# Optimization experiments

Hardware: AMD Instinct MI355X
Metric: run time of the kernel (lower is better)

Reference implementation:

```python
import jax, jax.numpy as jnp
import numpy as np

N_NODES = 100000
AVG_DEG = 32
E_UND = N_NODES * AVG_DEG // 2   # 1.6M undirected edges
E_DIR = 2 * E_UND                # 3.2M directed edges
Q = 4                            # number of communities
NUM_ITER = 10                    # max_num_iter in bp_params


def setup_inputs() -> dict:
    key = jax.random.key(0)
    k1, k2, k3, k4 = jax.random.split(key, 4)
    src_u = jax.random.randint(k1, (E_UND,), 0, N_NODES)
    dst_u = jax.random.randint(k2, (E_UND,), 0, N_NODES)
    # symmetric directed edge list: [forward block | reverse block]
    edge_index = jnp.stack([
        jnp.concatenate([src_u, dst_u]),
        jnp.concatenate([dst_u, src_u]),
    ]).astype(jnp.int64)
    w_u = jax.random.uniform(k3, (E_UND,), dtype=jnp.float32)
    edge_attr = jnp.concatenate([w_u, w_u])  # symmetric weights
    msg_init = jax.random.uniform(k4, (E_DIR, Q), dtype=jnp.float32) + 0.1
    # critical beta for q groups, mean degree c: log(q/(sqrt(c)-1)+1)
    beta = jnp.asarray(np.log(Q / (np.sqrt(AVG_DEG) - 1.0) + 1.0), dtype=jnp.float32)
    return {"edge_index": edge_index, "edge_attr": edge_attr,
            "msg_init": msg_init, "beta": beta, "num_nodes": N_NODES}


def _bp_forward(edge_index, edge_attr, msg_init, beta, num_nodes):
    q = msg_init.shape[1]
    E = edge_index.shape[1]
    e_und = E // 2
    src, dst = edge_index[0], edge_index[1]
    # reverse-edge permutation: edge e <-> e +/- e_und
    rev = jnp.concatenate([jnp.arange(e_und) + e_und, jnp.arange(e_und)])

    two_m = jnp.sum(edge_attr)                                   # = 2m (directed sum)
    deg = jax.ops.segment_sum(edge_attr, src, num_segments=num_nodes)  # weighted degree [N]
    expm1_bw = jnp.expm1(beta * edge_attr)[:, None]              # [E,1]

    psi0 = msg_init / jnp.sum(msg_init, axis=-1, keepdims=True)  # normalized cavity msgs [E,q]
    h0 = jnp.zeros((q,), dtype=msg_init.dtype)                   # external field

    def step(carry, _):
        psi, h = carry
        L = jnp.log1p(psi * expm1_bw)                            # [E,q] log(1 + psi*(e^{bw}-1))
        S = jax.ops.segment_sum(L, dst, num_segments=num_nodes)  # [N,q] incoming log-products
        marg = jax.nn.softmax(h[None, :] + S, axis=-1)           # node marginals [N,q]
        h_new = -(beta / two_m) * jnp.sum(deg[:, None] * marg, axis=0)  # [q]
        # cavity update for edge i->j: all incoming at i except reverse edge j->i
        msg_log = h_new[None, :] + S[src] - L[rev]
        psi_new = jax.nn.softmax(msg_log, axis=-1)
        return (psi_new, h_new), None

    (psi, h), _ = jax.lax.scan(step, (psi0, h0), None, length=NUM_ITER)

    # final node marginals s
    L = jnp.log1p(psi * expm1_bw)
    S = jax.ops.segment_sum(L, dst, num_segments=num_nodes)
    s = jax.nn.softmax(h[None, :] + S, axis=-1)                  # [N,q]

    # modularity: Q = (1/2m) sum_e w_e <s_i, s_j> - sum_t (sum_i d_i s_it / 2m)^2
    link = jnp.sum(edge_attr[:, None] * s[src] * s[dst]) / two_m
    comm_deg = jnp.sum(deg[:, None] * s, axis=0) / two_m         # [q]
    q_mod = link - jnp.sum(comm_deg * comm_deg)
    return s, q_mod


def reference(edge_index, edge_attr, msg_init, beta, num_nodes):
    return _bp_forward(edge_index, edge_attr, msg_init, beta, num_nodes)
```

## Files before the change

kernel.cpp:

```cpp
#include <hip/hip_runtime.h>


#define NBLK 256
#define QD 4
#define SENT 0x7fffffff

__device__ __forceinline__ float wave_red(float v) {
#pragma unroll
  for (int o = 32; o > 0; o >>= 1) v += __shfl_down(v, o, 64);
  return v;
}

__device__ __forceinline__ void atomicMulF(float* addr, float val) {
  unsigned int old = __float_as_uint(*addr), assumed;
  do {
    assumed = old;
    float nv = __uint_as_float(assumed) * val;
    old = atomicCAS((unsigned int*)addr, assumed, __float_as_uint(nv));
  } while (old != assumed);
}

__global__ void hist_rank(const int* __restrict__ ei, int* __restrict__ cnt,
                          int* __restrict__ rank, int E) {
  int G = gridDim.x * blockDim.x;
  int e[8], d[8];
#pragma unroll
  for (int j = 0; j < 8; ++j) {
    e[j] = blockIdx.x * blockDim.x + threadIdx.x + j * G;
    d[j] = (e[j] < E) ? ei[E + e[j]] : 0;
  }
#pragma unroll
  for (int j = 0; j < 8; ++j)
    if (e[j] < E) rank[e[j]] = atomicAdd(&cnt[d[j]], 1);
}

__global__ void scanA(const int* __restrict__ cnt, int* __restrict__ out,
                      int* __restrict__ bsum, int N) {
  __shared__ int lds[256];
  int base = blockIdx.x * 1024 + threadIdx.x * 4;
  int v0 = (base + 0 < N) ? cnt[base + 0] : 0;
  int v1 = (base + 1 < N) ? cnt[base + 1] : 0;
  int v2 = (base + 2 < N) ? cnt[base + 2] : 0;
  int v3 = (base + 3 < N) ? cnt[base + 3] : 0;
  lds[threadIdx.x] = v0 + v1 + v2 + v3;
  __syncthreads();
  for (int off = 1; off < 256; off <<= 1) {
    int x = (threadIdx.x >= off) ? lds[threadIdx.x - off] : 0;
    __syncthreads();
    if (threadIdx.x >= off) lds[threadIdx.x] += x;
    __syncthreads();
  }
  int excl = (threadIdx.x == 0) ? 0 : lds[threadIdx.x - 1];
  if (threadIdx.x == 255) bsum[blockIdx.x] = lds[255];
  if (base + 0 < N) out[base + 0] = excl;
  if (base + 1 < N) out[base + 1] = excl + v0;
  if (base + 2 < N) out[base + 2] = excl + v0 + v1;
  if (base + 3 < N) out[base + 3] = excl + v0 + v1 + v2;
}

__global__ void scanB(int* __restrict__ bsum, int NB) {
  __shared__ int lds[256];
  int v = (threadIdx.x < NB) ? bsum[threadIdx.x] : 0;
  lds[threadIdx.x] = v;
  __syncthreads();
  for (int off = 1; off < 256; off <<= 1) {
    int x = (threadIdx.x >= off) ? lds[threadIdx.x - off] : 0;
    __syncthreads();
    if (threadIdx.x >= off) lds[threadIdx.x] += x;
    __syncthreads();
  }
  int excl = (threadIdx.x == 0) ? 0 : lds[threadIdx.x - 1];
  if (threadIdx.x < NB) bsum[threadIdx.x] = excl;
}

__global__ void scanC(int* __restrict__ rowStart, const int* __restrict__ bsum,
                      int N, int E) {
  int i = blockIdx.x * blockDim.x + threadIdx.x;
  if (i < N) rowStart[i] += bsum[i >> 10];
  if (i == 0) rowStart[N] = E;
}

__global__ void scatter_inc(const int* __restrict__ ei, const int* __restrict__ rowStart,
                            const int* __restrict__ rank, int* __restrict__ inc, int E) {
  int G = gridDim.x * blockDim.x;
#pragma unroll
  for (int j = 0; j < 4; ++j) {
    int e = blockIdx.x * blockDim.x + threadIdx.x + j * G;
    if (e < E) {
      int d = ei[E + e];
      inc[rowStart[d] + rank[e]] = e;
    }
  }
}

__global__ void build_nodeOf(const int* __restrict__ rowStart, int* __restrict__ nodeOf,
                             int N) {
  int n = blockIdx.x * blockDim.x + threadIdx.x;
  if (n >= N) return;
  int s = rowStart[n], e = rowStart[n + 1];
  for (int k = s; k < e; ++k) nodeOf[k] = n;
}

__global__ void setup_pairs(const float* __restrict__ w, const float* __restrict__ msg,
                            const float* __restrict__ beta_p, float* __restrict__ F,
                            float* __restrict__ em_buf, double* __restrict__ two_m,
                            int Eh) {
  __shared__ float blk[4];
  int t = blockIdx.x * blockDim.x + threadIdx.x;
  float tw = 0.f;
  if (t < Eh) {
    float beta = beta_p[0];
    float wv = w[t];
    tw = 2.f * wv;
    float em = expm1f(beta * wv);
    em_buf[t] = em;
    float4 m1 = *reinterpret_cast<const float4*>(&msg[(size_t)t * QD]);
    float4 m2 = *reinterpret_cast<const float4*>(&msg[((size_t)t + Eh) * QD]);
    float i1 = em / (m1.x + m1.y + m1.z + m1.w);
    float i2 = em / (m2.x + m2.y + m2.z + m2.w);
    float4 F1 = make_float4(fmaf(m1.x, i1, 1.f), fmaf(m1.y, i1, 1.f),
                            fmaf(m1.z, i1, 1.f), fmaf(m1.w, i1, 1.f));
    float4 F2 = make_float4(fmaf(m2.x, i2, 1.f), fmaf(m2.y, i2, 1.f),
                            fmaf(m2.z, i2, 1.f), fmaf(m2.w, i2, 1.f));
    *reinterpret_cast<float4*>(&F[(size_t)t * QD]) = F1;
    *reinterpret_cast<float4*>(&F[((size_t)t + Eh) * QD]) = F2;
  }
  tw = wave_red(tw);
  int wid = threadIdx.x >> 6;
  if ((threadIdx.x & 63) == 0) blk[wid] = tw;
  __syncthreads();
  if (threadIdx.x == 0)
    atomicAdd(two_m, (double)(blk[0] + blk[1] + blk[2] + blk[3]));
}

__global__ void fillP(float* __restrict__ P, int n4) {
  int i = blockIdx.x * blockDim.x + threadIdx.x;
  if (i < n4) P[i] = 1.0f;
}

template <int NC, bool PROD, int NW>
__global__ void gather_seg(const int* __restrict__ inc, const int* __restrict__ nodeOf,
                           const float* __restrict__ src, float* __restrict__ out,
                           int E) {
  const int lane = threadIdx.x & 63;
  const int wid = threadIdx.x >> 6;
  const long long base = ((long long)blockIdx.x * (blockDim.x >> 6) + wid) * (NW * 64);
  if (base >= E) return;
  const float IDENT = PROD ? 1.f : 0.f;
  int n[NW], idx[NW];
  float v[NW][NC];
#pragma unroll
  for (int w = 0; w < NW; ++w) {
    long long k = base + w * 64 + lane;
    n[w] = (k < E) ? nodeOf[k] : SENT;
    idx[w] = (k < E) ? inc[k] : 0;
  }
#pragma unroll
  for (int w = 0; w < NW; ++w) {
    long long k = base + w * 64 + lane;
    if (k < E) {
      if constexpr (NC == 4) {
        float4 t = *reinterpret_cast<const float4*>(&src[(size_t)idx[w] * 4]);
        v[w][0] = t.x; v[w][1] = t.y; v[w][2] = t.z; v[w][3] = t.w;
      } else {
        v[w][0] = src[idx[w]];
      }
    } else {
#pragma unroll
      for (int c = 0; c < NC; ++c) v[w][c] = IDENT;
    }
  }
  int n00 = __shfl(n[0], 0, 64);
  int prevn = (base > 0) ? nodeOf[base - 1] : -1;
  const int incomplete = (prevn == n00) ? n00 : -1;
  int nwf[NW];
#pragma unroll
  for (int w = 0; w < NW - 1; ++w) nwf[w] = __shfl(n[w + 1], 0, 64);
  nwf[NW - 1] = (base + NW * 64 < E) ? nodeOf[base + NW * 64] : -1;

  float cv[NC];
#pragma unroll
  for (int c = 0; c < NC; ++c) cv[c] = IDENT;
  int cn = -1;
#pragma unroll
  for (int w = 0; w < NW; ++w) {
    int nn = n[w];
#pragma unroll
    for (int d = 1; d < 64; d <<= 1) {
      int pn = __shfl_up(nn, d, 64);
      float pv[NC];
#pragma unroll
      for (int c = 0; c < NC; ++c) pv[c] = __shfl_up(v[w][c], d, 64);
      if (lane >= d && pn == nn) {
#pragma unroll
        for (int c = 0; c < NC; ++c) {
          if constexpr (PROD) v[w][c] *= pv[c]; else v[w][c] += pv[c];
        }
      }
    }
    if (nn == cn) {
#pragma unroll
      for (int c = 0; c < NC; ++c) {
        if constexpr (PROD) v[w][c] *= cv[c]; else v[w][c] += cv[c];
      }
    }
    int nnext = __shfl_down(nn, 1, 64);
    if (lane == 63) nnext = nwf[w];
    bool segend = (nn != SENT) && (nnext != nn);
    if (segend) {
      if (nn == incomplete) {
#pragma unroll
        for (int c = 0; c < NC; ++c) {
          if constexpr (PROD) atomicMulF(&out[(size_t)nn * NC + c], v[w][c]);
          else atomicAdd(&out[(size_t)nn * NC + c], v[w][c]);
        }
      } else {
        if constexpr (NC == 4) {
          *reinterpret_cast<float4*>(&out[(size_t)nn * 4]) =
              make_float4(v[w][0], v[w][1], v[w][2], v[w][3]);
        } else {
          out[nn] = v[w][0];
        }
      }
    }
    int last_n = __shfl(nn, 63, 64);
    float lv[NC];
#pragma unroll
    for (int c = 0; c < NC; ++c) lv[c] = __shfl(v[w][c], 63, 64);
    bool last_end = (nwf[w] != last_n) || (last_n == SENT);
    if (last_end) {
      cn = -1;
#pragma unroll
      for (int c = 0; c < NC; ++c) cv[c] = IDENT;
    } else {
      cn = last_n;
#pragma unroll
      for (int c = 0; c < NC; ++c) cv[c] = lv[c];
    }
  }
  if (cn != -1 && lane == 0) {
#pragma unroll
    for (int c = 0; c < NC; ++c) {
      if constexpr (PROD) atomicMulF(&out[(size_t)cn * NC + c], cv[c]);
      else atomicAdd(&out[(size_t)cn * NC + c], cv[c]);
    }
  }
}

__global__ void node_post(const float* __restrict__ P, const float* __restrict__ deg,
                          const double* __restrict__ hsum_prev, double* __restrict__ hsum_new,
                          const float* __restrict__ beta_p, const double* __restrict__ two_m,
                          int N) {
  __shared__ float blk[4][4];
  int n = blockIdx.x * blockDim.x + threadIdx.x;
  float scale = -beta_p[0] / (float)two_m[0];
  float e0 = expf(scale * (float)hsum_prev[0]);
  float e1 = expf(scale * (float)hsum_prev[1]);
  float e2 = expf(scale * (float)hsum_prev[2]);
  float e3 = expf(scale * (float)hsum_prev[3]);
  float a0 = 0.f, a1 = 0.f, a2 = 0.f, a3 = 0.f;
  if (n < N) {
    float4 Pv = *reinterpret_cast<const float4*>(&P[(size_t)n * QD]);
    float m0 = e0 * Pv.x, m1 = e1 * Pv.y, m2 = e2 * Pv.z, m3 = e3 * Pv.w;
    float dinv = deg[n] / (m0 + m1 + m2 + m3);
    a0 = m0 * dinv; a1 = m1 * dinv; a2 = m2 * dinv; a3 = m3 * dinv;
  }
  a0 = wave_red(a0); a1 = wave_red(a1); a2 = wave_red(a2); a3 = wave_red(a3);
  int wid = threadIdx.x >> 6;
  if ((threadIdx.x & 63) == 0) {
    blk[wid][0] = a0; blk[wid][1] = a1; blk[wid][2] = a2; blk[wid][3] = a3;
  }
  __syncthreads();
  if (threadIdx.x < 4) {
    float s = blk[0][threadIdx.x] + blk[1][threadIdx.x] + blk[2][threadIdx.x] +
              blk[3][threadIdx.x];
    atomicAdd(&hsum_new[threadIdx.x], (double)s);
  }
}

__global__ void node_post_final(const float* __restrict__ P, const float* __restrict__ deg,
                                const double* __restrict__ hsum, const float* __restrict__ beta_p,
                                const double* __restrict__ two_m, float* __restrict__ out_s,
                                double* __restrict__ comm_raw, int N) {
  __shared__ float blk[4][4];
  int n = blockIdx.x * blockDim.x + threadIdx.x;
  float scale = -beta_p[0] / (float)two_m[0];
  float e0 = expf(scale * (float)hsum[0]);
  float e1 = expf(scale * (float)hsum[1]);
  float e2 = expf(scale * (float)hsum[2]);
  float e3 = expf(scale * (float)hsum[3]);
  float a0 = 0.f, a1 = 0.f, a2 = 0.f, a3 = 0.f;
  if (n < N) {
    float4 Pv = *reinterpret_cast<const float4*>(&P[(size_t)n * QD]);
    float m0 = e0 * Pv.x, m1 = e1 * Pv.y, m2 = e2 * Pv.z, m3 = e3 * Pv.w;
    float inv = 1.f / (m0 + m1 + m2 + m3);
    float4 s = make_float4(m0 * inv, m1 * inv, m2 * inv, m3 * inv);
    *reinterpret_cast<float4*>(&out_s[(size_t)n * QD]) = s;
    float d = deg[n];
    a0 = d * s.x; a1 = d * s.y; a2 = d * s.z; a3 = d * s.w;
  }
  a0 = wave_red(a0); a1 = wave_red(a1); a2 = wave_red(a2); a3 = wave_red(a3);
  int wid = threadIdx.x >> 6;
  if ((threadIdx.x & 63) == 0) {
    blk[wid][0] = a0; blk[wid][1] = a1; blk[wid][2] = a2; blk[wid][3] = a3;
  }
  __syncthreads();
  if (threadIdx.x < 4) {
    float s = blk[0][threadIdx.x] + blk[1][threadIdx.x] + blk[2][threadIdx.x] +
              blk[3][threadIdx.x];
    atomicAdd(&comm_raw[threadIdx.x], (double)s);
  }
}

__global__ void edge_fuse(const int* __restrict__ ei, const float* __restrict__ em_buf,
                          const float* __restrict__ P, float* __restrict__ F,
                          const double* __restrict__ hsum, const float* __restrict__ beta_p,
                          const double* __restrict__ two_m, int E, int Eh) {
  int t = blockIdx.x * blockDim.x + threadIdx.x;
  if (t >= Eh) return;
  float scale = -beta_p[0] / (float)two_m[0];
  float e0 = expf(scale * (float)hsum[0]);
  float e1 = expf(scale * (float)hsum[1]);
  float e2 = expf(scale * (float)hsum[2]);
  float e3 = expf(scale * (float)hsum[3]);
  int s1 = ei[t];
  int d1 = ei[E + t];
  float em = em_buf[t];
  float4 F1 = *reinterpret_cast<const float4*>(&F[(size_t)t * QD]);
  float4 F2 = *reinterpret_cast<const float4*>(&F[((size_t)t + Eh) * QD]);
  float4 Ps = *reinterpret_cast<const float4*>(&P[(size_t)s1 * QD]);
  float4 Pd = *reinterpret_cast<const float4*>(&P[(size_t)d1 * QD]);
  {
    float a01 = F2.x * F2.y, a23 = F2.z * F2.w;
    float x0 = F2.y * a23, x1 = F2.x * a23, x2 = a01 * F2.w, x3 = a01 * F2.z;
    float n0 = e0 * Ps.x * x0, n1 = e1 * Ps.y * x1;
    float n2 = e2 * Ps.z * x2, n3 = e3 * Ps.w * x3;
    float tt = em / (n0 + n1 + n2 + n3);
    float4 Fn = make_float4(fmaf(n0, tt, 1.f), fmaf(n1, tt, 1.f),
                            fmaf(n2, tt, 1.f), fmaf(n3, tt, 1.f));
    *reinterpret_cast<float4*>(&F[(size_t)t * QD]) = Fn;
  }
  {
    float a01 = F1.x * F1.y, a23 = F1.z * F1.w;
    float x0 = F1.y * a23, x1 = F1.x * a23, x2 = a01 * F1.w, x3 = a01 * F1.z;
    float n0 = e0 * Pd.x * x0, n1 = e1 * Pd.y * x1;
    float n2 = e2 * Pd.z * x2, n3 = e3 * Pd.w * x3;
    float tt = em / (n0 + n1 + n2 + n3);
    float4 Fn = make_float4(fmaf(n0, tt, 1.f), fmaf(n1, tt, 1.f),
                            fmaf(n2, tt, 1.f), fmaf(n3, tt, 1.f));
    *reinterpret_cast<float4*>(&F[((size_t)t + Eh) * QD]) = Fn;
  }
}

__global__ void edge_final(const int* __restrict__ ei, const float* __restrict__ w,
                           const float* __restrict__ out_s,
                           double* __restrict__ link_raw, int E, int Eh) {
  __shared__ float blk[4];
  int G = gridDim.x * blockDim.x;
  float c = 0.f;
  for (int t = blockIdx.x * blockDim.x + threadIdx.x; t < Eh; t += G) {
    int s1 = ei[t];
    int d1 = ei[E + t];
    float4 a = *reinterpret_cast<const float4*>(&out_s[(size_t)s1 * QD]);
    float4 b = *reinterpret_cast<const float4*>(&out_s[(size_t)d1 * QD]);
    float dot = a.x * b.x + a.y * b.y + a.z * b.z + a.w * b.w;
    c += 2.f * w[t] * dot;
  }
  c = wave_red(c);
  int wid = threadIdx.x >> 6;
  if ((threadIdx.x & 63) == 0) blk[wid] = c;
  __syncthreads();
  if (threadIdx.x == 0)
    atomicAdd(link_raw, (double)(blk[0] + blk[1] + blk[2] + blk[3]));
}

__global__ void finalize(const double* __restrict__ scal, float* __restrict__ out_q) {
  double tm = scal[0];
  double link = scal[1] / tm;
  double acc = 0.0;
#pragma unroll
  for (int k = 0; k < QD; ++k) {
    double c = scal[2 + k] / tm;
    acc += c * c;
  }
  out_q[0] = (float)(link - acc);
}

extern "C" void kernel_launch(void* const* d_in, const int* in_sizes, int n_in,
                              void* d_out, int out_size, void* d_ws, size_t ws_size,
                              hipStream_t stream) {
  const int* ei = (const int*)d_in[0];
  const float* w = (const float*)d_in[1];
  const float* msg = (const float*)d_in[2];
  const float* beta_p = (const float*)d_in[3];

  const int E = in_sizes[1];
  const int Eh = E / 2;
  const int N = (out_size - 1) / QD;

  char* p = (char*)d_ws;
  double* scal = (double*)p;
  size_t off = 512;
  int* cnt = (int*)(p + off); off += (size_t)N * 4;
  int* rowStart = (int*)(p + off); off += (size_t)(N + 1) * 4;
  off = (off + 127) & ~(size_t)127;
  int* bsum = (int*)(p + off); off += 1024;
  int* inc = (int*)(p + off); off += (size_t)E * 4;
  float* deg = (float*)(p + off); off += (size_t)N * 4;
  off = (off + 15) & ~(size_t)15;
  float* P = (float*)(p + off); off += (size_t)N * QD * 4;
  float* em = (float*)(p + off); off += (size_t)Eh * 4;
  off = (off + 15) & ~(size_t)15;
  float* F = (float*)(p + off); off += (size_t)E * QD * 4;
  int* rank = (int*)F;
  int* nodeOf = (int*)(p + off); off += (size_t)E * 4;
  (void)ws_size;

  double* hs = scal + 6;
  const int gEdir = (E + NBLK - 1) / NBLK;
  const int gE = (Eh + NBLK - 1) / NBLK;
  const int gN = (N + NBLK - 1) / NBLK;
  const int gH = (E + NBLK * 8 - 1) / (NBLK * 8);
  const int gSc = (E + NBLK * 4 - 1) / (NBLK * 4);
  const int gWp = (E + 2047) / 2048;
  const int gWd = (E + 1023) / 1024;
  const int gF = (4 * N + NBLK - 1) / NBLK;
  const int NBscan = (N + 1023) / 1024;

  hipMemsetAsync(scal, 0, 512, stream);
  hipMemsetAsync(cnt, 0, (size_t)N * 4, stream);
  hipMemsetAsync(deg, 0, (size_t)N * 4, stream);

  hist_rank<<<gH, NBLK, 0, stream>>>(ei, cnt, rank, E);
  scanA<<<NBscan, 256, 0, stream>>>(cnt, rowStart, bsum, N);
  scanB<<<1, 256, 0, stream>>>(bsum, NBscan);
  scanC<<<(N + NBLK) / NBLK, NBLK, 0, stream>>>(rowStart, bsum, N, E);
  scatter_inc<<<gSc, NBLK, 0, stream>>>(ei, rowStart, rank, inc, E);
  build_nodeOf<<<gN, NBLK, 0, stream>>>(rowStart, nodeOf, N);

  setup_pairs<<<gE, NBLK, 0, stream>>>(w, msg, beta_p, F, em, scal, Eh);
  gather_seg<1, false, 4><<<gWd, NBLK, 0, stream>>>(inc, nodeOf, w, deg, E);

  float* out_s = (float*)d_out;
  for (int i = 1; i <= 10; ++i) {
    fillP<<<gF, NBLK, 0, stream>>>(P, 4 * N);
    gather_seg<4, true, 8><<<gWp, NBLK, 0, stream>>>(inc, nodeOf, F, P, E);
    node_post<<<gN, NBLK, 0, stream>>>(P, deg, hs + 4 * (i - 1), hs + 4 * i,
                                       beta_p, scal, N);
    edge_fuse<<<gE, NBLK, 0, stream>>>(ei, em, P, F, hs + 4 * i, beta_p, scal, E, Eh);
  }
  fillP<<<gF, NBLK, 0, stream>>>(P, 4 * N);
  gather_seg<4, true, 8><<<gWp, NBLK, 0, stream>>>(inc, nodeOf, F, P, E);
  node_post_final<<<gN, NBLK, 0, stream>>>(P, deg, hs + 40, beta_p, scal,
                                           out_s, scal + 2, N);
  edge_final<<<512, NBLK, 0, stream>>>(ei, w, out_s, scal + 1, E, Eh);
  finalize<<<1, 1, 0, stream>>>(scal, out_s + (size_t)N * QD);
}
```

Measured before the change: 1.719 ms.

## Split F gather into separate permute pass and double edge work per thread

Adds a gatherF kernel that permutes edge messages into destination-sorted order (Fg) with 8 independent loads per thread. The segmented product then reads Fg sequentially instead of through the incidence index, but only when the workspace is large enough. edge_fuse now processes two edge pairs per thread over half the grid, and scatter_inc handles 8 edges per thread. The cost is an extra full E×4 float write and read per iteration plus an extra kernel launch.

```diff
diff --git a/kernel.cpp b/kernel.cpp
--- a/kernel.cpp
+++ b/kernel.cpp
@@ -84,7 +84,7 @@
                             const int* __restrict__ rank, int* __restrict__ inc, int E) {
   int G = gridDim.x * blockDim.x;
 #pragma unroll
-  for (int j = 0; j < 4; ++j) {
+  for (int j = 0; j < 8; ++j) {
     int e = blockIdx.x * blockDim.x + threadIdx.x + j * G;
     if (e < E) {
       int d = ei[E + e];
@@ -138,7 +138,25 @@
   if (i < n4) P[i] = 1.0f;
 }
 
-template <int NC, bool PROD, int NW>
+__global__ void gatherF(const int* __restrict__ inc, const float* __restrict__ F,
+                        float* __restrict__ Fg, int E) {
+  int G = gridDim.x * blockDim.x;
+  int k[8], id[8];
+#pragma unroll
+  for (int j = 0; j < 8; ++j) {
+    k[j] = blockIdx.x * blockDim.x + threadIdx.x + j * G;
+    id[j] = (k[j] < E) ? inc[k[j]] : 0;
+  }
+  float4 v[8];
+#pragma unroll
+  for (int j = 0; j < 8; ++j)
+    v[j] = *reinterpret_cast<const float4*>(&F[(size_t)id[j] * QD]);
+#pragma unroll
+  for (int j = 0; j < 8; ++j)
+    if (k[j] < E) *reinterpret_cast<float4*>(&Fg[(size_t)k[j] * QD]) = v[j];
+}
+
+template <int NC, bool PROD, int NW, bool SEQIDX>
 __global__ void gather_seg(const int* __restrict__ inc, const int* __restrict__ nodeOf,
                            const float* __restrict__ src, float* __restrict__ out,
                            int E) {
@@ -153,7 +171,8 @@
   for (int w = 0; w < NW; ++w) {
     long long k = base + w * 64 + lane;
     n[w] = (k < E) ? nodeOf[k] : SENT;
-    idx[w] = (k < E) ? inc[k] : 0;
+    if constexpr (SEQIDX) idx[w] = (int)k;
+    else idx[w] = (k < E) ? inc[k] : 0;
   }
 #pragma unroll
   for (int w = 0; w < NW; ++w) {
@@ -316,40 +335,52 @@
                           const float* __restrict__ P, float* __restrict__ F,
                           const double* __restrict__ hsum, const float* __restrict__ beta_p,
                           const double* __restrict__ two_m, int E, int Eh) {
-  int t = blockIdx.x * blockDim.x + threadIdx.x;
-  if (t >= Eh) return;
+  int G = gridDim.x * blockDim.x;
+  int t0 = blockIdx.x * blockDim.x + threadIdx.x;
+  int t1 = t0 + G;
   float scale = -beta_p[0] / (float)two_m[0];
   float e0 = expf(scale * (float)hsum[0]);
   float e1 = expf(scale * (float)hsum[1]);
   float e2 = expf(scale * (float)hsum[2]);
   float e3 = expf(scale * (float)hsum[3]);
-  int s1 = ei[t];
-  int d1 = ei[E + t];
-  float em = em_buf[t];
-  float4 F1 = *reinterpret_cast<const float4*>(&F[(size_t)t * QD]);
-  float4 F2 = *reinterpret_cast<const float4*>(&F[((size_t)t + Eh) * QD]);
-  float4 Ps = *reinterpret_cast<const float4*>(&P[(size_t)s1 * QD]);
-  float4 Pd = *reinterpret_cast<const float4*>(&P[(size_t)d1 * QD]);
-  {
-    float a01 = F2.x * F2.y, a23 = F2.z * F2.w;
-    float x0 = F2.y * a23, x1 = F2.x * a23, x2 = a01 * F2.w, x3 = a01 * F2.z;
-    float n0 = e0 * Ps.x * x0, n1 = e1 * Ps.y * x1;
-    float n2 = e2 * Ps.z * x2, n3 = e3 * Ps.w * x3;
-    float tt = em / (n0 + n1 + n2 + n3);
-    float4 Fn = make_float4(fmaf(n0, tt, 1.f), fmaf(n1, tt, 1.f),
-                            fmaf(n2, tt, 1.f), fmaf(n3, tt, 1.f));
-    *reinterpret_cast<float4*>(&F[(size_t)t * QD]) = Fn;
-  }
-  {
-    float a01 = F1.x * F1.y, a23 = F1.z * F1.w;
-    float x0 = F1.y * a23, x1 = F1.x * a23, x2 = a01 * F1.w, x3 = a01 * F1.z;
-    float n0 = e0 * Pd.x * x0, n1 = e1 * Pd.y * x1;
-    float n2 = e2 * Pd.z * x2, n3 = e3 * Pd.w * x3;
-    float tt = em / (n0 + n1 + n2 + n3);
-    float4 Fn = make_float4(fmaf(n0, tt, 1.f), fmaf(n1, tt, 1.f),
-                            fmaf(n2, tt, 1.f), fmaf(n3, tt, 1.f));
-    *reinterpret_cast<float4*>(&F[((size_t)t + Eh) * QD]) = Fn;
-  }
+  int s1a = 0, d1a = 0, s1b = 0, d1b = 0;
+  float ema = 0.f, emb = 0.f;
+  if (t0 < Eh) { s1a = ei[t0]; d1a = ei[E + t0]; ema = em_buf[t0]; }
+  if (t1 < Eh) { s1b = ei[t1]; d1b = ei[E + t1]; emb = em_buf[t1]; }
+  float4 F1a, F2a, F1b, F2b, Psa, Pda, Psb, Pdb;
+  if (t0 < Eh) {
+    F1a = *reinterpret_cast<const float4*>(&F[(size_t)t0 * QD]);
+    F2a = *reinterpret_cast<const float4*>(&F[((size_t)t0 + Eh) * QD]);
+    Psa = *reinterpret_cast<const float4*>(&P[(size_t)s1a * QD]);
+    Pda = *reinterpret_cast<const float4*>(&P[(size_t)d1a * QD]);
+  }
+  if (t1 < Eh) {
+    F1b = *reinterpret_cast<const float4*>(&F[(size_t)t1 * QD]);
+    F2b = *reinterpret_cast<const float4*>(&F[((size_t)t1 + Eh) * QD]);
+    Psb = *reinterpret_cast<const float4*>(&P[(size_t)s1b * QD]);
+    Pdb = *reinterpret_cast<const float4*>(&P[(size_t)d1b * QD]);
+  }
+#define CAV(Fr, Pn, em, dstp)                                            \
+  {                                                                      \
+    float a01 = (Fr).x * (Fr).y, a23 = (Fr).z * (Fr).w;                  \
+    float x0 = (Fr).y * a23, x1 = (Fr).x * a23;                          \
+    float x2 = a01 * (Fr).w, x3 = a01 * (Fr).z;                          \
+    float n0 = e0 * (Pn).x * x0, n1 = e1 * (Pn).y * x1;                  \
+    float n2 = e2 * (Pn).z * x2, n3 = e3 * (Pn).w * x3;                  \
+    float tt = (em) / (n0 + n1 + n2 + n3);                               \
+    *reinterpret_cast<float4*>(dstp) =                                   \
+        make_float4(fmaf(n0, tt, 1.f), fmaf(n1, tt, 1.f),                \
+                    fmaf(n2, tt, 1.f), fmaf(n3, tt, 1.f));               \
+  }
+  if (t0 < Eh) {
+    CAV(F2a, Psa, ema, &F[(size_t)t0 * QD]);
+    CAV(F1a, Pda, ema, &F[((size_t)t0 + Eh) * QD]);
+  }
+  if (t1 < Eh) {
+    CAV(F2b, Psb, emb, &F[(size_t)t1 * QD]);
+    CAV(F1b, Pdb, emb, &F[((size_t)t1 + Eh) * QD]);
+  }
+#undef CAV
 }
 
 __global__ void edge_final(const int* __restrict__ ei, const float* __restrict__ w,
@@ -414,14 +445,17 @@
   float* F = (float*)(p + off); off += (size_t)E * QD * 4;
   int* rank = (int*)F;
   int* nodeOf = (int*)(p + off); off += (size_t)E * 4;
-  (void)ws_size;
+  off = (off + 15) & ~(size_t)15;
+  float* Fg = (float*)(p + off); off += (size_t)E * QD * 4;
+  const bool twophase = ws_size >= off;
 
   double* hs = scal + 6;
   const int gEdir = (E + NBLK - 1) / NBLK;
   const int gE = (Eh + NBLK - 1) / NBLK;
+  const int gE2 = (Eh / 2 + NBLK - 1) / NBLK + 1;
   const int gN = (N + NBLK - 1) / NBLK;
   const int gH = (E + NBLK * 8 - 1) / (NBLK * 8);
-  const int gSc = (E + NBLK * 4 - 1) / (NBLK * 4);
+  const int gGF = (E + NBLK * 8 - 1) / (NBLK * 8);
   const int gWp = (E + 2047) / 2048;
   const int gWd = (E + 1023) / 1024;
   const int gF = (4 * N + NBLK - 1) / NBLK;
@@ -435,22 +469,27 @@
   scanA<<<NBscan, 256, 0, stream>>>(cnt, rowStart, bsum, N);
   scanB<<<1, 256, 0, stream>>>(bsum, NBscan);
   scanC<<<(N + NBLK) / NBLK, NBLK, 0, stream>>>(rowStart, bsum, N, E);
-  scatter_inc<<<gSc, NBLK, 0, stream>>>(ei, rowStart, rank, inc, E);
+  scatter_inc<<<gH, NBLK, 0, stream>>>(ei, rowStart, rank, inc, E);
   build_nodeOf<<<gN, NBLK, 0, stream>>>(rowStart, nodeOf, N);
 
   setup_pairs<<<gE, NBLK, 0, stream>>>(w, msg, beta_p, F, em, scal, Eh);
-  gather_seg<1, false, 4><<<gWd, NBLK, 0, stream>>>(inc, nodeOf, w, deg, E);
+  gather_seg<1, false, 4, false><<<gWd, NBLK, 0, stream>>>(inc, nodeOf, w, deg, E);
 
   float* out_s = (float*)d_out;
-  for (int i = 1; i <= 10; ++i) {
+  for (int i = 1; i <= 11; ++i) {
     fillP<<<gF, NBLK, 0, stream>>>(P, 4 * N);
-    gather_seg<4, true, 8><<<gWp, NBLK, 0, stream>>>(inc, nodeOf, F, P, E);
-    node_post<<<gN, NBLK, 0, stream>>>(P, deg, hs + 4 * (i - 1), hs + 4 * i,
-                                       beta_p, scal, N);
-    edge_fuse<<<gE, NBLK, 0, stream>>>(ei, em, P, F, hs + 4 * i, beta_p, scal, E, Eh);
-  }
-  fillP<<<gF, NBLK, 0, stream>>>(P, 4 * N);
-  gather_seg<4, true, 8><<<gWp, NBLK, 0, stream>>>(inc, nodeOf, F, P, E);
+    if (twophase) {
+      gatherF<<<gGF, NBLK, 0, stream>>>(inc, F, Fg, E);
+      gather_seg<4, true, 8, true><<<gWp, NBLK, 0, stream>>>(inc, nodeOf, Fg, P, E);
+    } else {
+      gather_seg<4, true, 8, false><<<gWp, NBLK, 0, stream>>>(inc, nodeOf, F, P, E);
+    }
+    if (i <= 10) {
+      node_post<<<gN, NBLK, 0, stream>>>(P, deg, hs + 4 * (i - 1), hs + 4 * i,
+                                         beta_p, scal, N);
+      edge_fuse<<<gE2, NBLK, 0, stream>>>(ei, em, P, F, hs + 4 * i, beta_p, scal, E, Eh);
+    }
+  }
   node_post_final<<<gN, NBLK, 0, stream>>>(P, deg, hs + 40, beta_p, scal,
                                            out_s, scal + 2, N);
   edge_final<<<512, NBLK, 0, stream>>>(ei, w, out_s, scal + 1, E, Eh);
```

After: 1.954 ms. 1.14x slower.

## Store cavity messages in CSR order with double-buffered per-slot metadata

Applied to the files above, without the earlier changes.

Edge messages F are now kept in destination-sorted CSR order, so the product-gather reads F sequentially instead of through the inc indirection. A setup kernel precomputes, per CSR slot, the source node, the edge weight term and the slot of the reverse edge. A new cavity kernel writes F_new in CSR order using the reverse slot, with ping-pong buffers to avoid read/write hazards. The cost is extra workspace and random reads of the reverse edge's F in the cavity step; the old path stays as a fallback when the workspace is too small.

```diff
diff --git a/kernel.cpp b/kernel.cpp
--- a/kernel.cpp
+++ b/kernel.cpp
@@ -80,15 +80,18 @@
   if (i == 0) rowStart[N] = E;
 }
 
-__global__ void scatter_inc(const int* __restrict__ ei, const int* __restrict__ rowStart,
-                            const int* __restrict__ rank, int* __restrict__ inc, int E) {
+__global__ void scatter_inc2(const int* __restrict__ ei, const int* __restrict__ rowStart,
+                             const int* __restrict__ rank, int* __restrict__ inc,
+                             int* __restrict__ csrPos, int E) {
   int G = gridDim.x * blockDim.x;
 #pragma unroll
   for (int j = 0; j < 4; ++j) {
     int e = blockIdx.x * blockDim.x + threadIdx.x + j * G;
     if (e < E) {
       int d = ei[E + e];
-      inc[rowStart[d] + rank[e]] = e;
+      int pos = rowStart[d] + rank[e];
+      inc[pos] = e;
+      csrPos[e] = pos;
     }
   }
 }
@@ -104,7 +107,7 @@
 __global__ void setup_pairs(const float* __restrict__ w, const float* __restrict__ msg,
                             const float* __restrict__ beta_p, float* __restrict__ F,
                             float* __restrict__ em_buf, double* __restrict__ two_m,
-                            int Eh) {
+                            int Eh, int writeF) {
   __shared__ float blk[4];
   int t = blockIdx.x * blockDim.x + threadIdx.x;
   float tw = 0.f;
@@ -114,16 +117,18 @@
     tw = 2.f * wv;
     float em = expm1f(beta * wv);
     em_buf[t] = em;
-    float4 m1 = *reinterpret_cast<const float4*>(&msg[(size_t)t * QD]);
-    float4 m2 = *reinterpret_cast<const float4*>(&msg[((size_t)t + Eh) * QD]);
-    float i1 = em / (m1.x + m1.y + m1.z + m1.w);
-    float i2 = em / (m2.x + m2.y + m2.z + m2.w);
-    float4 F1 = make_float4(fmaf(m1.x, i1, 1.f), fmaf(m1.y, i1, 1.f),
-                            fmaf(m1.z, i1, 1.f), fmaf(m1.w, i1, 1.f));
-    float4 F2 = make_float4(fmaf(m2.x, i2, 1.f), fmaf(m2.y, i2, 1.f),
-                            fmaf(m2.z, i2, 1.f), fmaf(m2.w, i2, 1.f));
-    *reinterpret_cast<float4*>(&F[(size_t)t * QD]) = F1;
-    *reinterpret_cast<float4*>(&F[((size_t)t + Eh) * QD]) = F2;
+    if (writeF) {
+      float4 m1 = *reinterpret_cast<const float4*>(&msg[(size_t)t * QD]);
+      float4 m2 = *reinterpret_cast<const float4*>(&msg[((size_t)t + Eh) * QD]);
+      float i1 = em / (m1.x + m1.y + m1.z + m1.w);
+      float i2 = em / (m2.x + m2.y + m2.z + m2.w);
+      float4 F1 = make_float4(fmaf(m1.x, i1, 1.f), fmaf(m1.y, i1, 1.f),
+                              fmaf(m1.z, i1, 1.f), fmaf(m1.w, i1, 1.f));
+      float4 F2 = make_float4(fmaf(m2.x, i2, 1.f), fmaf(m2.y, i2, 1.f),
+                              fmaf(m2.z, i2, 1.f), fmaf(m2.w, i2, 1.f));
+      *reinterpret_cast<float4*>(&F[(size_t)t * QD]) = F1;
+      *reinterpret_cast<float4*>(&F[((size_t)t + Eh) * QD]) = F2;
+    }
   }
   tw = wave_red(tw);
   int wid = threadIdx.x >> 6;
@@ -133,12 +138,37 @@
     atomicAdd(two_m, (double)(blk[0] + blk[1] + blk[2] + blk[3]));
 }
 
+__global__ void build_csrmeta(const int* __restrict__ inc, const int* __restrict__ csrPos,
+                              const int* __restrict__ ei, const float* __restrict__ em,
+                              const float* __restrict__ msg, int* __restrict__ srcOf,
+                              float* __restrict__ em_csr, int* __restrict__ revslot,
+                              float* __restrict__ F0csr, int E, int Eh) {
+  int G = gridDim.x * blockDim.x;
+#pragma unroll
+  for (int j = 0; j < 4; ++j) {
+    int k = blockIdx.x * blockDim.x + threadIdx.x + j * G;
+    if (k >= E) continue;
+    int e = inc[k];
+    int pr = (e < Eh) ? e : e - Eh;
+    int re = (e < Eh) ? e + Eh : e - Eh;
+    float emv = em[pr];
+    srcOf[k] = ei[e];
+    em_csr[k] = emv;
+    revslot[k] = csrPos[re];
+    float4 m = *reinterpret_cast<const float4*>(&msg[(size_t)e * QD]);
+    float i1 = emv / (m.x + m.y + m.z + m.w);
+    *reinterpret_cast<float4*>(&F0csr[(size_t)k * QD]) =
+        make_float4(fmaf(m.x, i1, 1.f), fmaf(m.y, i1, 1.f),
+                    fmaf(m.z, i1, 1.f), fmaf(m.w, i1, 1.f));
+  }
+}
+
 __global__ void fillP(float* __restrict__ P, int n4) {
   int i = blockIdx.x * blockDim.x + threadIdx.x;
   if (i < n4) P[i] = 1.0f;
 }
 
-template <int NC, bool PROD, int NW>
+template <int NC, bool PROD, int NW, bool SEQIDX>
 __global__ void gather_seg(const int* __restrict__ inc, const int* __restrict__ nodeOf,
                            const float* __restrict__ src, float* __restrict__ out,
                            int E) {
@@ -153,7 +183,8 @@
   for (int w = 0; w < NW; ++w) {
     long long k = base + w * 64 + lane;
     n[w] = (k < E) ? nodeOf[k] : SENT;
-    idx[w] = (k < E) ? inc[k] : 0;
+    if constexpr (SEQIDX) idx[w] = (int)k;
+    else idx[w] = (k < E) ? inc[k] : 0;
   }
 #pragma unroll
   for (int w = 0; w < NW; ++w) {
@@ -247,68 +278,45 @@
   }
 }
 
-__global__ void node_post(const float* __restrict__ P, const float* __restrict__ deg,
-                          const double* __restrict__ hsum_prev, double* __restrict__ hsum_new,
-                          const float* __restrict__ beta_p, const double* __restrict__ two_m,
-                          int N) {
-  __shared__ float blk[4][4];
-  int n = blockIdx.x * blockDim.x + threadIdx.x;
-  float scale = -beta_p[0] / (float)two_m[0];
-  float e0 = expf(scale * (float)hsum_prev[0]);
-  float e1 = expf(scale * (float)hsum_prev[1]);
-  float e2 = expf(scale * (float)hsum_prev[2]);
-  float e3 = expf(scale * (float)hsum_prev[3]);
-  float a0 = 0.f, a1 = 0.f, a2 = 0.f, a3 = 0.f;
-  if (n < N) {
-    float4 Pv = *reinterpret_cast<const float4*>(&P[(size_t)n * QD]);
-    float m0 = e0 * Pv.x, m1 = e1 * Pv.y, m2 = e2 * Pv.z, m3 = e3 * Pv.w;
-    float dinv = deg[n] / (m0 + m1 + m2 + m3);
-    a0 = m0 * dinv; a1 = m1 * dinv; a2 = m2 * dinv; a3 = m3 * dinv;
-  }
-  a0 = wave_red(a0); a1 = wave_red(a1); a2 = wave_red(a2); a3 = wave_red(a3);
-  int wid = threadIdx.x >> 6;
-  if ((threadIdx.x & 63) == 0) {
-    blk[wid][0] = a0; blk[wid][1] = a1; blk[wid][2] = a2; blk[wid][3] = a3;
-  }
-  __syncthreads();
-  if (threadIdx.x < 4) {
-    float s = blk[0][threadIdx.x] + blk[1][threadIdx.x] + blk[2][threadIdx.x] +
-              blk[3][threadIdx.x];
-    atomicAdd(&hsum_new[threadIdx.x], (double)s);
-  }
-}
-
-__global__ void node_post_final(const float* __restrict__ P, const float* __restrict__ deg,
-                                const double* __restrict__ hsum, const float* __restrict__ beta_p,
-                                const double* __restrict__ two_m, float* __restrict__ out_s,
-                                double* __restrict__ comm_raw, int N) {
-  __shared__ float blk[4][4];
-  int n = blockIdx.x * blockDim.x + threadIdx.x;
+__global__ void cavity_csr(const int* __restrict__ srcOf, const int* __restrict__ revslot,
+                           const float* __restrict__ em_csr, const float* __restrict__ P,
+                           const float* __restrict__ F_old, float* __restrict__ F_new,
+                           const double* __restrict__ hsum, const float* __restrict__ beta_p,
+                           const double* __restrict__ two_m, int E) {
+  int G = gridDim.x * blockDim.x;
   float scale = -beta_p[0] / (float)two_m[0];
   float e0 = expf(scale * (float)hsum[0]);
   float e1 = expf(scale * (float)hsum[1]);
   float e2 = expf(scale * (float)hsum[2]);
   float e3 = expf(scale * (float)hsum[3]);
-  float a0 = 0.f, a1 = 0.f, a2 = 0.f, a3 = 0.f;
-  if (n < N) {
-    float4 Pv = *reinterpret_cast<const float4*>(&P[(size_t)n * QD]);
-    float m0 = e0 * Pv.x, m1 = e1 * Pv.y, m2 = e2 * Pv.z, m3 = e3 * Pv.w;
-    float inv = 1.f / (m0 + m1 + m2 + m3);
-    float4 s = make_float4(m0 * inv, m1 * inv, m2 * inv, m3 * inv);
-    *reinterpret_cast<float4*>(&out_s[(size_t)n * QD]) = s;
-    float d = deg[n];
-    a0 = d * s.x; a1 = d * s.y; a2 = d * s.z; a3 = d * s.w;
-  }
-  a0 = wave_red(a0); a1 = wave_red(a1); a2 = wave_red(a2); a3 = wave_red(a3);
-  int wid = threadIdx.x >> 6;
-  if ((threadIdx.x & 63) == 0) {
-    blk[wid][0] = a0; blk[wid][1] = a1; blk[wid][2] = a2; blk[wid][3] = a3;
-  }
-  __syncthreads();
-  if (threadIdx.x < 4) {
-    float s = blk[0][threadIdx.x] + blk[1][threadIdx.x] + blk[2][threadIdx.x] +
-              blk[3][threadIdx.x];
-    atomicAdd(&comm_raw[threadIdx.x], (double)s);
+  int k[4], rs[4], sc[4];
+  float emv[4];
+#pragma unroll
+  for (int j = 0; j < 4; ++j) {
+    k[j] = blockIdx.x * blockDim.x + threadIdx.x + j * G;
+    bool ok = k[j] < E;
+    rs[j] = ok ? revslot[k[j]] : 0;
+    sc[j] = ok ? srcOf[k[j]] : 0;
+    emv[j] = ok ? em_csr[k[j]] : 0.f;
+  }
+  float4 Fr[4], Ps[4];
+#pragma unroll
+  for (int j = 0; j < 4; ++j) {
+    Fr[j] = *reinterpret_cast<const float4*>(&F_old[(size_t)rs[j] * QD]);
+    Ps[j] = *reinterpret_cast<const float4*>(&P[(size_t)sc[j] * QD]);
+  }
+#pragma unroll
+  for (int j = 0; j < 4; ++j) {
+    if (k[j] >= E) continue;
+    float a01 = Fr[j].x * Fr[j].y, a23 = Fr[j].z * Fr[j].w;
+    float x0 = Fr[j].y * a23, x1 = Fr[j].x * a23;
+    float x2 = a01 * Fr[j].w, x3 = a01 * Fr[j].z;
+    float n0 = e0 * Ps[j].x * x0, n1 = e1 * Ps[j].y * x1;
+    float n2 = e2 * Ps[j].z * x2, n3 = e3 * Ps[j].w * x3;
+    float tt = emv[j] / (n0 + n1 + n2 + n3);
+    *reinterpret_cast<float4*>(&F_new[(size_t)k[j] * QD]) =
+        make_float4(fmaf(n0, tt, 1.f), fmaf(n1, tt, 1.f),
+                    fmaf(n2, tt, 1.f), fmaf(n3, tt, 1.f));
   }
 }
 
@@ -336,9 +344,9 @@
     float n0 = e0 * Ps.x * x0, n1 = e1 * Ps.y * x1;
     float n2 = e2 * Ps.z * x2, n3 = e3 * Ps.w * x3;
     float tt = em / (n0 + n1 + n2 + n3);
-    float4 Fn = make_float4(fmaf(n0, tt, 1.f), fmaf(n1, tt, 1.f),
-                            fmaf(n2, tt, 1.f), fmaf(n3, tt, 1.f));
-    *reinterpret_cast<float4*>(&F[(size_t)t * QD]) = Fn;
+    *reinterpret_cast<float4*>(&F[(size_t)t * QD]) =
+        make_float4(fmaf(n0, tt, 1.f), fmaf(n1, tt, 1.f),
+                    fmaf(n2, tt, 1.f), fmaf(n3, tt, 1.f));
   }
   {
     float a01 = F1.x * F1.y, a23 = F1.z * F1.w;
@@ -346,9 +354,74 @@
     float n0 = e0 * Pd.x * x0, n1 = e1 * Pd.y * x1;
     float n2 = e2 * Pd.z * x2, n3 = e3 * Pd.w * x3;
     float tt = em / (n0 + n1 + n2 + n3);
-    float4 Fn = make_float4(fmaf(n0, tt, 1.f), fmaf(n1, tt, 1.f),
-                            fmaf(n2, tt, 1.f), fmaf(n3, tt, 1.f));
-    *reinterpret_cast<float4*>(&F[((size_t)t + Eh) * QD]) = Fn;
+    *reinterpret_cast<float4*>(&F[((size_t)t + Eh) * QD]) =
+        make_float4(fmaf(n0, tt, 1.f), fmaf(n1, tt, 1.f),
+                    fmaf(n2, tt, 1.f), fmaf(n3, tt, 1.f));
+  }
+}
+
+__global__ void node_post(const float* __restrict__ P, const float* __restrict__ deg,
+                          const double* __restrict__ hsum_prev, double* __restrict__ hsum_new,
+                          const float* __restrict__ beta_p, const double* __restrict__ two_m,
+                          int N) {
+  __shared__ float blk[4][4];
+  int n = blockIdx.x * blockDim.x + threadIdx.x;
+  float scale = -beta_p[0] / (float)two_m[0];
+  float e0 = expf(scale * (float)hsum_prev[0]);
+  float e1 = expf(scale * (float)hsum_prev[1]);
+  float e2 = expf(scale * (float)hsum_prev[2]);
+  float e3 = expf(scale * (float)hsum_prev[3]);
+  float a0 = 0.f, a1 = 0.f, a2 = 0.f, a3 = 0.f;
+  if (n < N) {
+    float4 Pv = *reinterpret_cast<const float4*>(&P[(size_t)n * QD]);
+    float m0 = e0 * Pv.x, m1 = e1 * Pv.y, m2 = e2 * Pv.z, m3 = e3 * Pv.w;
+    float dinv = deg[n] / (m0 + m1 + m2 + m3);
+    a0 = m0 * dinv; a1 = m1 * dinv; a2 = m2 * dinv; a3 = m3 * dinv;
+  }
+  a0 = wave_red(a0); a1 = wave_red(a1); a2 = wave_red(a2); a3 = wave_red(a3);
+  int wid = threadIdx.x >> 6;
+  if ((threadIdx.x & 63) == 0) {
+    blk[wid][0] = a0; blk[wid][1] = a1; blk[wid][2] = a2; blk[wid][3] = a3;
+  }
+  __syncthreads();
+  if (threadIdx.x < 4) {
+    float s = blk[0][threadIdx.x] + blk[1][threadIdx.x] + blk[2][threadIdx.x] +
+              blk[3][threadIdx.x];
+    atomicAdd(&hsum_new[threadIdx.x], (double)s);
+  }
+}
+
+__global__ void node_post_final(const float* __restrict__ P, const float* __restrict__ deg,
+                                const double* __restrict__ hsum, const float* __restrict__ beta_p,
+                                const double* __restrict__ two_m, float* __restrict__ out_s,
+                                double* __restrict__ comm_raw, int N) {
+  __shared__ float blk[4][4];
+  int n = blockIdx.x * blockDim.x + threadIdx.x;
+  float scale = -beta_p[0] / (float)two_m[0];
+  float e0 = expf(scale * (float)hsum[0]);
+  float e1 = expf(scale * (float)hsum[1]);
+  float e2 = expf(scale * (float)hsum[2]);
+  float e3 = expf(scale * (float)hsum[3]);
+  float a0 = 0.f, a1 = 0.f, a2 = 0.f, a3 = 0.f;
+  if (n < N) {
+    float4 Pv = *reinterpret_cast<const float4*>(&P[(size_t)n * QD]);
+    float m0 = e0 * Pv.x, m1 = e1 * Pv.y, m2 = e2 * Pv.z, m3 = e3 * Pv.w;
+    float inv = 1.f / (m0 + m1 + m2 + m3);
+    float4 s = make_float4(m0 * inv, m1 * inv, m2 * inv, m3 * inv);
+    *reinterpret_cast<float4*>(&out_s[(size_t)n * QD]) = s;
+    float d = deg[n];
+    a0 = d * s.x; a1 = d * s.y; a2 = d * s.z; a3 = d * s.w;
+  }
+  a0 = wave_red(a0); a1 = wave_red(a1); a2 = wave_red(a2); a3 = wave_red(a3);
+  int wid = threadIdx.x >> 6;
+  if ((threadIdx.x & 63) == 0) {
+    blk[wid][0] = a0; blk[wid][1] = a1; blk[wid][2] = a2; blk[wid][3] = a3;
+  }
+  __syncthreads();
+  if (threadIdx.x < 4) {
+    float s = blk[0][threadIdx.x] + blk[1][threadIdx.x] + blk[2][threadIdx.x] +
+              blk[3][threadIdx.x];
+    atomicAdd(&comm_raw[threadIdx.x], (double)s);
   }
 }
 
@@ -405,25 +478,32 @@
   int* rowStart = (int*)(p + off); off += (size_t)(N + 1) * 4;
   off = (off + 127) & ~(size_t)127;
   int* bsum = (int*)(p + off); off += 1024;
-  int* inc = (int*)(p + off); off += (size_t)E * 4;
   float* deg = (float*)(p + off); off += (size_t)N * 4;
   off = (off + 15) & ~(size_t)15;
   float* P = (float*)(p + off); off += (size_t)N * QD * 4;
   float* em = (float*)(p + off); off += (size_t)Eh * 4;
+  int* nodeOf = (int*)(p + off); off += (size_t)E * 4;
+  int* srcOf = (int*)(p + off); off += (size_t)E * 4;
+  float* em_csr = (float*)(p + off); off += (size_t)E * 4;
+  int* revslot = (int*)(p + off); off += (size_t)E * 4;
   off = (off + 15) & ~(size_t)15;
-  float* F = (float*)(p + off); off += (size_t)E * QD * 4;
-  int* rank = (int*)F;
-  int* nodeOf = (int*)(p + off); off += (size_t)E * 4;
-  (void)ws_size;
+  float* F_A = (float*)(p + off); off += (size_t)E * QD * 4;
+  size_t offB = off;
+  float* F_B = (float*)(p + off); off += (size_t)E * QD * 4;
+  int* rank = (int*)F_A;
+  int* csrPos = (int*)F_B;
+  int* inc = (int*)F_B + E;
+  const size_t need_fallback = offB + (size_t)2 * E * 4;
+  const bool v2 = ws_size >= off;
+  (void)need_fallback;
 
   double* hs = scal + 6;
-  const int gEdir = (E + NBLK - 1) / NBLK;
   const int gE = (Eh + NBLK - 1) / NBLK;
   const int gN = (N + NBLK - 1) / NBLK;
   const int gH = (E + NBLK * 8 - 1) / (NBLK * 8);
-  const int gSc = (E + NBLK * 4 - 1) / (NBLK * 4);
+  const int gS4 = (E + NBLK * 4 - 1) / (NBLK * 4);
+  const int gWs = (E + 1023) / 1024;
   const int gWp = (E + 2047) / 2048;
-  const int gWd = (E + 1023) / 1024;
   const int gF = (4 * N + NBLK - 1) / NBLK;
   const int NBscan = (N + 1023) / 1024;
 
@@ -435,22 +515,37 @@
   scanA<<<NBscan, 256, 0, stream>>>(cnt, rowStart, bsum, N);
   scanB<<<1, 256, 0, stream>>>(bsum, NBscan);
   scanC<<<(N + NBLK) / NBLK, NBLK, 0, stream>>>(rowStart, bsum, N, E);
-  scatter_inc<<<gSc, NBLK, 0, stream>>>(ei, rowStart, rank, inc, E);
+  scatter_inc2<<<gS4, NBLK, 0, stream>>>(ei, rowStart, rank, inc, csrPos, E);
   build_nodeOf<<<gN, NBLK, 0, stream>>>(rowStart, nodeOf, N);
 
-  setup_pairs<<<gE, NBLK, 0, stream>>>(w, msg, beta_p, F, em, scal, Eh);
-  gather_seg<1, false, 4><<<gWd, NBLK, 0, stream>>>(inc, nodeOf, w, deg, E);
+  setup_pairs<<<gE, NBLK, 0, stream>>>(w, msg, beta_p, F_A, em, scal, Eh, v2 ? 0 : 1);
+  if (v2)
+    build_csrmeta<<<gS4, NBLK, 0, stream>>>(inc, csrPos, ei, em, msg, srcOf,
+                                            em_csr, revslot, F_A, E, Eh);
+  gather_seg<1, false, 4, false><<<gWs, NBLK, 0, stream>>>(inc, nodeOf, w, deg, E);
 
   float* out_s = (float*)d_out;
-  for (int i = 1; i <= 10; ++i) {
+  float* Fc = F_A;
+  float* Fn = F_B;
+  for (int i = 1; i <= 11; ++i) {
     fillP<<<gF, NBLK, 0, stream>>>(P, 4 * N);
-    gather_seg<4, true, 8><<<gWp, NBLK, 0, stream>>>(inc, nodeOf, F, P, E);
-    node_post<<<gN, NBLK, 0, stream>>>(P, deg, hs + 4 * (i - 1), hs + 4 * i,
-                                       beta_p, scal, N);
-    edge_fuse<<<gE, NBLK, 0, stream>>>(ei, em, P, F, hs + 4 * i, beta_p, scal, E, Eh);
-  }
-  fillP<<<gF, NBLK, 0, stream>>>(P, 4 * N);
-  gather_seg<4, true, 8><<<gWp, NBLK, 0, stream>>>(inc, nodeOf, F, P, E);
+    if (v2)
+      gather_seg<4, true, 4, true><<<gWs, NBLK, 0, stream>>>(inc, nodeOf, Fc, P, E);
+    else
+      gather_seg<4, true, 8, false><<<gWp, NBLK, 0, stream>>>(inc, nodeOf, F_A, P, E);
+    if (i <= 10) {
+      node_post<<<gN, NBLK, 0, stream>>>(P, deg, hs + 4 * (i - 1), hs + 4 * i,
+                                         beta_p, scal, N);
+      if (v2) {
+        cavity_csr<<<gS4, NBLK, 0, stream>>>(srcOf, revslot, em_csr, P, Fc, Fn,
+                                             hs + 4 * i, beta_p, scal, E);
+        float* tmp = Fc; Fc = Fn; Fn = tmp;
+      } else {
+        edge_fuse<<<gE, NBLK, 0, stream>>>(ei, em, P, F_A, hs + 4 * i, beta_p,
+                                           scal, E, Eh);
+      }
+    }
+  }
   node_post_final<<<gN, NBLK, 0, stream>>>(P, deg, hs + 40, beta_p, scal,
                                            out_s, scal + 2, N);
   edge_final<<<512, NBLK, 0, stream>>>(ei, w, out_s, scal + 1, E, Eh);
```

Result: slower. 1.948 ms (+13.3%).
